# Performance work log

Hardware: AMD Instinct MI355X
Metric: run time of the kernel (lower is better)

Reference implementation:

```python
import jax, jax.numpy as jnp
import numpy as np

FORGET_BIAS = 1.0
LAYERS = 2


def setup_inputs() -> dict:
    key = jax.random.key(0)
    ks = jax.random.split(key, 10)
    B, T, H, V = 64, 50, 256, 50000
    G = 4 * H
    s = 1.0 / np.sqrt(H)
    return {
        "input_data": jax.random.randint(ks[0], (B, T), 0, V, dtype=jnp.int64),
        "embedding": jax.random.uniform(ks[1], (V, H), jnp.float32, -1.0, 1.0),
        "Wx": jax.random.normal(ks[2], (LAYERS, H, G), jnp.float32) * s,
        "Uh": jax.random.normal(ks[3], (LAYERS, H, G), jnp.float32) * s,
        "alpha": jax.random.uniform(ks[4], (LAYERS, G), jnp.float32),
        "beta1": jax.random.uniform(ks[5], (LAYERS, G), jnp.float32),
        "beta2": jax.random.uniform(ks[6], (LAYERS, G), jnp.float32),
        "bias": jnp.zeros((LAYERS, G), jnp.float32),
        "softmax_w": jax.random.normal(ks[7], (V, H), jnp.float32) * s,
        "softmax_b": jnp.full((V,), 0.1, jnp.float32),
    }


def _mi_lstm_stack(inputs_tbh, Wx, Uh, alpha, beta1, beta2, bias):
    # inputs_tbh: [T, B, H]; params have leading layer axis [L, ...]
    T, B, H = inputs_tbh.shape
    c0 = jnp.zeros((LAYERS, B, H), inputs_tbh.dtype)
    h0 = jnp.zeros((LAYERS, B, H), inputs_tbh.dtype)

    def step(carry, x_t):
        c, h = carry
        inp = x_t
        new_c, new_h = [], []
        for l in range(LAYERS):
            xh = inp @ Wx[l]          # [B, 4H]
            hh = h[l] @ Uh[l]         # [B, 4H]
            gates = alpha[l] * xh * hh + beta1[l] * xh + beta2[l] * hh + bias[l]
            i, j, f, o = jnp.split(gates, 4, axis=-1)
            c_l = c[l] * jax.nn.sigmoid(f + FORGET_BIAS) + jax.nn.sigmoid(i) * jnp.tanh(j)
            h_l = jnp.tanh(c_l) * jax.nn.sigmoid(o)
            new_c.append(c_l)
            new_h.append(h_l)
            inp = h_l
        return (jnp.stack(new_c), jnp.stack(new_h)), inp

    (_, _), outs = jax.lax.scan(step, (c0, h0), inputs_tbh)
    return outs  # [T, B, H] top-layer hidden states


def reference(input_data, embedding, Wx, Uh, alpha, beta1, beta2, bias, softmax_w, softmax_b):
    # embedding lookup: [B, T, H] -> time-major [T, B, H]
    x = embedding[input_data]
    outs = _mi_lstm_stack(jnp.transpose(x, (1, 0, 2)), Wx, Uh, alpha, beta1, beta2, bias)
    # batch-major flatten like tf.reshape(outputs, [-1, rnn_size]) on [B, T, H]
    H = outs.shape[-1]
    flat = jnp.transpose(outs, (1, 0, 2)).reshape(-1, H)  # [B*T, H]
    logits = flat @ softmax_w.T + softmax_b               # [B*T, V]
    return logits
```

## Files before the change

### kernel.cpp

```cpp
#include <hip/hip_runtime.h>
#include <hip/hip_bf16.h>
#include <math.h>

#define B_ 64
#define T_ 50
#define H_ 256
#define G_ 1024
#define V_ 50000
#define NBLK 32
#define BSTRIDE 64

using f16x8 = __attribute__((ext_vector_type(8))) _Float16;
using f16x4 = __attribute__((ext_vector_type(4))) _Float16;
using f32x4 = __attribute__((ext_vector_type(4))) float;

__device__ __forceinline__ float sigm(float x) { return 1.0f / (1.0f + expf(-x)); }

__global__ __launch_bounds__(64) void embed_k(const int* __restrict__ idx,
                                              const float* __restrict__ emb,
                                              _Float16* __restrict__ x16)
{
    const int row = blockIdx.x;
    const int b = row & (B_ - 1);
    const int t = row >> 6;
    const int id = idx[b * T_ + t];
    const float4 v = *reinterpret_cast<const float4*>(emb + (size_t)id * H_ + threadIdx.x * 4);
    f16x4 h;
    h[0] = (_Float16)v.x; h[1] = (_Float16)v.y;
    h[2] = (_Float16)v.z; h[3] = (_Float16)v.w;
    *reinterpret_cast<f16x4*>(x16 + (size_t)row * H_ + threadIdx.x * 4) = h;
}

__global__ __launch_bounds__(256) void conv_half(const float* __restrict__ in,
                                                 _Float16* __restrict__ out, int n)
{
    const int i = (blockIdx.x * 256 + threadIdx.x) * 8;
    if (i + 8 <= n) {
        const float4 v0 = *reinterpret_cast<const float4*>(in + i);
        const float4 v1 = *reinterpret_cast<const float4*>(in + i + 4);
        f16x8 h;
        h[0] = (_Float16)v0.x; h[1] = (_Float16)v0.y;
        h[2] = (_Float16)v0.z; h[3] = (_Float16)v0.w;
        h[4] = (_Float16)v1.x; h[5] = (_Float16)v1.y;
        h[6] = (_Float16)v1.z; h[7] = (_Float16)v1.w;
        *reinterpret_cast<f16x8*>(out + i) = h;
    }
}

__global__ __launch_bounds__(256) void pack_wx0(const float* __restrict__ Wx0,
                                                _Float16* __restrict__ wxT)
{
    __shared__ _Float16 ts[64][65];
    const int k0 = blockIdx.x * 64;
    const int n0 = blockIdx.y * 64;
    const int tr = threadIdx.x >> 6;
    const int tc = threadIdx.x & 63;
#pragma unroll
    for (int i = 0; i < 16; ++i) {
        const int r = i * 4 + tr;
        ts[r][tc] = (_Float16)Wx0[(size_t)(k0 + r) * G_ + n0 + tc];
    }
    __syncthreads();
#pragma unroll
    for (int i = 0; i < 16; ++i) {
        const int c = i * 4 + tr;
        wxT[(size_t)(n0 + c) * H_ + k0 + tc] = ts[tc][c];
    }
}

__global__ __launch_bounds__(256) void pack_w_rec(const float* __restrict__ Uh0,
                                                  const float* __restrict__ Wx1,
                                                  const float* __restrict__ Uh1,
                                                  _Float16* __restrict__ wpk)
{
    const int c = blockIdx.x;
    const int m = blockIdx.y;
    const float* __restrict__ src = (m == 0) ? Uh0 : (m == 1) ? Wx1 : Uh1;
    _Float16* __restrict__ dst = wpk + (((size_t)c * 3 + m) << 13);
    for (int i = threadIdx.x; i < 8192; i += 256) {
        const int k = i >> 5;
        const int col = i & 31;
        const int colg = ((col >> 3) << 8) + (c << 3) + (col & 7);
        dst[(col << 8) + k] = (_Float16)src[(size_t)k * G_ + colg];
    }
}

__device__ __forceinline__ void gload_lds16(const void* g, void* l)
{
    __builtin_amdgcn_global_load_lds(
        (const __attribute__((address_space(1))) unsigned int*)g,
        (__attribute__((address_space(3))) unsigned int*)l, 16, 0, 0);
}

__device__ __forceinline__ void gbar_arrive(int* slot)
{
    __syncthreads();
    if (threadIdx.x == 0) {
        __threadfence();
        __hip_atomic_fetch_add(slot, 1, __ATOMIC_RELAXED, __HIP_MEMORY_SCOPE_AGENT);
    }
}

__device__ __forceinline__ void gbar_wait_fast(int* slot)
{
    if (threadIdx.x == 0) {
        while (__hip_atomic_load(slot, __ATOMIC_RELAXED, __HIP_MEMORY_SCOPE_AGENT) < NBLK)
            __builtin_amdgcn_s_sleep(1);
    }
    __syncthreads();
    __threadfence();
}

#define PM 128
#define PN 128
#define PK 64

__global__ __launch_bounds__(256) void gemm16_mfma(
    const _Float16* __restrict__ A16,
    const _Float16* __restrict__ B16,
    float* __restrict__ C)
{
    __shared__ __align__(16) _Float16 Asub[PM * PK];
    __shared__ __align__(16) _Float16 Bsub[PN * PK];

    const int tid = threadIdx.x;
    const int l = tid & 63;
    const int w = tid >> 6;
    const int wm = w >> 1, wn = w & 1;

    const int n0 = blockIdx.x * PN;
    const int m0 = blockIdx.y * PM;

    f32x4 acc[4][4] = {};

    for (int k0 = 0; k0 < H_; k0 += PK) {
#pragma unroll
        for (int is = 0; is < 4; ++is) {
            const int i = is * 256 + tid;
            const int r = i >> 3;
            const int ch = (i & 7) ^ (r & 7);
            gload_lds16(A16 + (size_t)(m0 + r) * H_ + k0 + ch * 8, &Asub[i * 8]);
            gload_lds16(B16 + (size_t)(n0 + r) * H_ + k0 + ch * 8, &Bsub[i * 8]);
        }
        __syncthreads();

#pragma unroll
        for (int ks = 0; ks < 2; ++ks) {
            f16x8 af[4], bf[4];
#pragma unroll
            for (int i = 0; i < 4; ++i) {
                const int r = wm * 64 + i * 16 + (l & 15);
                const int ch = (ks * 4 + (l >> 4)) ^ (r & 7);
                af[i] = *reinterpret_cast<const f16x8*>(&Asub[r * PK + ch * 8]);
            }
#pragma unroll
            for (int jf = 0; jf < 4; ++jf) {
                const int r = wn * 64 + jf * 16 + (l & 15);
                const int ch = (ks * 4 + (l >> 4)) ^ (r & 7);
                bf[jf] = *reinterpret_cast<const f16x8*>(&Bsub[r * PK + ch * 8]);
            }
#pragma unroll
            for (int i = 0; i < 4; ++i)
#pragma unroll
                for (int jf = 0; jf < 4; ++jf)
                    acc[i][jf] = __builtin_amdgcn_mfma_f32_16x16x32_f16(
                        af[i], bf[jf], acc[i][jf], 0, 0, 0);
        }
        __syncthreads();
    }

    const int rb = (l >> 4) << 2;
    const int cl = l & 15;
#pragma unroll
    for (int jf = 0; jf < 4; ++jf) {
        const int col = n0 + wn * 64 + jf * 16 + cl;
#pragma unroll
        for (int i = 0; i < 4; ++i) {
            const int rowb = m0 + wm * 64 + i * 16 + rb;
#pragma unroll
            for (int r = 0; r < 4; ++r)
                C[(size_t)(rowb + r) * G_ + col] = acc[i][jf][r];
        }
    }
}

__global__ __launch_bounds__(256) void mi_rec(
    const _Float16* __restrict__ wpk,
    const float* __restrict__ xh0,
    _Float16* __restrict__ h0x,
    _Float16* __restrict__ h1x,
    _Float16* __restrict__ outsH,
    int* __restrict__ bars,
    const float* __restrict__ alpha, const float* __restrict__ b1,
    const float* __restrict__ b2, const float* __restrict__ bsv)
{
    __shared__ __align__(16) _Float16 h0l[16384];
    __shared__ __align__(16) _Float16 h1l[16384];
    __shared__ __align__(16) _Float16 wl[24576];
    __shared__ float gA[2112], gB[2112];
    __shared__ float c0l[512], c1l[512];

    const int c = blockIdx.x;
    const int tid = threadIdx.x;
    const int l = tid & 63;
    const int w = tid >> 6;

    for (int i = tid; i < 2048; i += 256) {
        *reinterpret_cast<f16x8*>(&h0l[i << 3]) = f16x8{};
        *reinterpret_cast<f16x8*>(&h1l[i << 3]) = f16x8{};
    }
    for (int i = tid; i < 512; i += 256) { c0l[i] = 0.f; c1l[i] = 0.f; }

    for (int i = tid; i < 3072; i += 256) {
        const int m = i >> 10;
        const int col = (i >> 5) & 31;
        const int ch = i & 31;
        const f16x8 v = *reinterpret_cast<const f16x8*>(
            &wpk[(((size_t)c * 3 + m) * 32 + col) * 256 + (ch << 3)]);
        *reinterpret_cast<f16x8*>(
            &wl[(m * 32 + col) * 256 + ((ch ^ (col & 7)) << 3)]) = v;
    }

    const int u = tid & 7, b0 = tid >> 3;
    const int jl = (c << 3) + u;
    float al0[4], b10[4], b20[4], bs0[4], al1[4], b11[4], b21[4], bs1[4];
#pragma unroll
    for (int g = 0; g < 4; ++g) {
        const int col = (g << 8) + jl;
        al0[g] = alpha[col];        b10[g] = b1[col];
        b20[g] = b2[col];           bs0[g] = bsv[col];
        al1[g] = alpha[G_ + col];   b11[g] = b1[G_ + col];
        b21[g] = b2[G_ + col];      bs1[g] = bsv[G_ + col];
    }
    __syncthreads();

    const int arow = (w << 4) + (l & 15);
    const int cA = l & 15, cB = 16 + (l & 15);
    const int kq = l >> 4;

    auto MM = [&](const _Float16* am, const _Float16* bm, f32x4& A0, f32x4& A1) {
#pragma unroll
        for (int s = 0; s < 8; ++s) {
            const int ck = (s << 2) + kq;
            const f16x8 af = *reinterpret_cast<const f16x8*>(
                &am[(arow << 8) + ((ck ^ (arow & 7)) << 3)]);
            const f16x8 bf0 = *reinterpret_cast<const f16x8*>(
                &bm[(cA << 8) + ((ck ^ (cA & 7)) << 3)]);
            const f16x8 bf1 = *reinterpret_cast<const f16x8*>(
                &bm[(cB << 8) + ((ck ^ (cB & 7)) << 3)]);
            A0 = __builtin_amdgcn_mfma_f32_16x16x32_f16(af, bf0, A0, 0, 0, 0);
            A1 = __builtin_amdgcn_mfma_f32_16x16x32_f16(af, bf1, A1, 0, 0, 0);
        }
    };
    auto STG = [&](float* gl, f32x4 A0, f32x4 A1) {
        const int rb = (w << 4) + (kq << 2);
#pragma unroll
        for (int r = 0; r < 4; ++r) {
            gl[(rb + r) * 33 + cA] = A0[r];
            gl[(rb + r) * 33 + cB] = A1[r];
        }
    };
    auto STAGE_H = [&](const _Float16* src, _Float16* dst) {
#pragma unroll
        for (int it = 0; it < 8; ++it) {
            const int idx = (it << 8) + tid;
            const int row = idx >> 5, ch = idx & 31;
            const f16x8 v = *reinterpret_cast<const f16x8*>(&src[(row << 8) + (ch << 3)]);
            *reinterpret_cast<f16x8*>(&dst[(row << 8) + ((ch ^ (row & 7)) << 3)]) = v;
        }
    };

    for (int s = 0; s <= T_; ++s) {
        const int p = s & 1;
        _Float16* h0w = h0x + (p << 14);
        _Float16* h1w = h1x + (p << 14);

        if (s < T_) {
            f32x4 A0 = {}, A1 = {};
            MM(h0l, wl, A0, A1);
            STG(gA, A0, A1);
            __syncthreads();
#pragma unroll
            for (int bb = 0; bb < 2; ++bb) {
                const int b = b0 + (bb << 5);
                float g4[4];
#pragma unroll
                for (int g = 0; g < 4; ++g) {
                    const float a = gA[b * 33 + (g << 3) + u];
                    const float x = xh0[(((size_t)(s * B_ + b)) << 10) + (g << 8) + jl];
                    g4[g] = al0[g] * x * a + b10[g] * x + b20[g] * a + bs0[g];
                }
                const float cn = c0l[(b << 3) + u] * sigm(g4[2] + 1.f)
                               + sigm(g4[0]) * tanhf(g4[1]);
                c0l[(b << 3) + u] = cn;
                h0w[(b << 8) + jl] = (_Float16)(tanhf(cn) * sigm(g4[3]));
            }
            __syncthreads();
        }

        if (s > 0) {
            f32x4 X0 = {}, X1 = {}, H0 = {}, H1 = {};
            MM(h0l, wl + 1 * 8192, X0, X1);
            MM(h1l, wl + 2 * 8192, H0, H1);
            STG(gA, X0, X1);
            STG(gB, H0, H1);
            __syncthreads();
#pragma unroll
            for (int bb = 0; bb < 2; ++bb) {
                const int b = b0 + (bb << 5);
                float g4[4];
#pragma unroll
                for (int g = 0; g < 4; ++g) {
                    const float xa = gA[b * 33 + (g << 3) + u];
                    const float ha = gB[b * 33 + (g << 3) + u];
                    g4[g] = al1[g] * xa * ha + b11[g] * xa + b21[g] * ha + bs1[g];
                }
                const float cn = c1l[(b << 3) + u] * sigm(g4[2] + 1.f)
                               + sigm(g4[0]) * tanhf(g4[1]);
                c1l[(b << 3) + u] = cn;
                const float hn = tanhf(cn) * sigm(g4[3]);
                h1w[(b << 8) + jl] = (_Float16)hn;
                outsH[(((size_t)b * T_ + (s - 1)) << 8) + jl] = (_Float16)hn;
            }
        }

        if (s < T_) {
            gbar_arrive(bars + s * BSTRIDE);
            gbar_wait_fast(bars + s * BSTRIDE);
            STAGE_H(h0w, h0l);
            if (s > 0) STAGE_H(h1w, h1l);
            __syncthreads();
        }
    }
}

__global__ __launch_bounds__(256) void proj_mfma(
    const _Float16* __restrict__ A16,
    const _Float16* __restrict__ B16,
    const float* __restrict__ bias,
    float* __restrict__ C)
{
    __shared__ __align__(16) _Float16 Asub[PM * PK];
    __shared__ __align__(16) _Float16 Bsub[PN * PK];

    const int tid = threadIdx.x;
    const int l = tid & 63;
    const int w = tid >> 6;
    const int wm = w >> 1, wn = w & 1;

    const int m0 = blockIdx.x * PM;
    const int n0 = blockIdx.y * PN;

    f32x4 acc[4][4] = {};

    for (int k0 = 0; k0 < H_; k0 += PK) {
#pragma unroll
        for (int is = 0; is < 4; ++is) {
            const int i = is * 256 + tid;
            const int r = i >> 3;
            const int ch = (i & 7) ^ (r & 7);
            gload_lds16(A16 + (size_t)(m0 + r) * H_ + k0 + ch * 8, &Asub[i * 8]);
            int n = n0 + r; if (n > V_ - 1) n = V_ - 1;
            gload_lds16(B16 + (size_t)n * H_ + k0 + ch * 8, &Bsub[i * 8]);
        }
        __syncthreads();

#pragma unroll
        for (int ks = 0; ks < 2; ++ks) {
            f16x8 af[4], bf[4];
#pragma unroll
            for (int i = 0; i < 4; ++i) {
                const int r = wm * 64 + i * 16 + (l & 15);
                const int ch = (ks * 4 + (l >> 4)) ^ (r & 7);
                af[i] = *reinterpret_cast<const f16x8*>(&Asub[r * PK + ch * 8]);
            }
#pragma unroll
            for (int jf = 0; jf < 4; ++jf) {
                const int r = wn * 64 + jf * 16 + (l & 15);
                const int ch = (ks * 4 + (l >> 4)) ^ (r & 7);
                bf[jf] = *reinterpret_cast<const f16x8*>(&Bsub[r * PK + ch * 8]);
            }
#pragma unroll
            for (int i = 0; i < 4; ++i)
#pragma unroll
                for (int jf = 0; jf < 4; ++jf)
                    acc[i][jf] = __builtin_amdgcn_mfma_f32_16x16x32_f16(
                        af[i], bf[jf], acc[i][jf], 0, 0, 0);
        }
        __syncthreads();
    }

    const int rb = (l >> 4) << 2;
    const int cl = l & 15;
#pragma unroll
    for (int jf = 0; jf < 4; ++jf) {
        const int col = n0 + wn * 64 + jf * 16 + cl;
        if (col < V_) {
            const float bv = bias[col];
#pragma unroll
            for (int i = 0; i < 4; ++i) {
                const int rowb = m0 + wm * 64 + i * 16 + rb;
#pragma unroll
                for (int r = 0; r < 4; ++r)
                    C[(size_t)(rowb + r) * V_ + col] = acc[i][jf][r] + bv;
            }
        }
    }
}

extern "C" void kernel_launch(void* const* d_in, const int* in_sizes, int n_in,
                              void* d_out, int out_size, void* d_ws, size_t ws_size,
                              hipStream_t stream)
{
    const int*   idx   = (const int*)  d_in[0];
    const float* emb   = (const float*)d_in[1];
    const float* Wx    = (const float*)d_in[2];
    const float* Uh    = (const float*)d_in[3];
    const float* alpha = (const float*)d_in[4];
    const float* b1    = (const float*)d_in[5];
    const float* b2    = (const float*)d_in[6];
    const float* bsv   = (const float*)d_in[7];
    const float* sw    = (const float*)d_in[8];
    const float* sb    = (const float*)d_in[9];
    float* out = (float*)d_out;

    char* wsb = (char*)d_ws;
    _Float16* x16   = (_Float16*)(wsb);
    float*    xh0   = (float*)   (wsb + 1638400);
    _Float16* outsH = (_Float16*)(wsb + 14745600);
    _Float16* w16   = (_Float16*)(wsb + 16384000);
    _Float16* wxT   = (_Float16*)(wsb + 41984000);
    _Float16* wpk   = (_Float16*)(wsb + 42508288);
    _Float16* h0x   = (_Float16*)(wsb + 44081152);
    _Float16* h1x   = (_Float16*)(wsb + 44146688);
    int*      bars  = (int*)     (wsb + 44212224);

    const float* Wx0 = Wx;
    const float* Wx1 = Wx + (size_t)H_ * G_;
    const float* Uh0 = Uh;
    const float* Uh1 = Uh + (size_t)H_ * G_;

    (void)hipMemsetAsync(bars, 0, 16384, stream);

    {
        dim3 grid(NBLK, 3);
        pack_w_rec<<<grid, 256, 0, stream>>>(Uh0, Wx1, Uh1, wpk);
    }
    {
        dim3 grid(4, 16);
        pack_wx0<<<grid, 256, 0, stream>>>(Wx0, wxT);
    }
    conv_half<<<(V_ * H_) / 2048, 256, 0, stream>>>(sw, w16, V_ * H_);

    embed_k<<<T_ * B_, 64, 0, stream>>>(idx, emb, x16);

    {
        dim3 grid(G_ / PN, 3200 / PM);
        gemm16_mfma<<<grid, 256, 0, stream>>>(x16, wxT, xh0);
    }

    mi_rec<<<NBLK, 256, 0, stream>>>(wpk, xh0, h0x, h1x, outsH, bars,
                                     alpha, b1, b2, bsv);

    {
        dim3 grid(3200 / PM, (V_ + PN - 1) / PN);
        proj_mfma<<<grid, 256, 0, stream>>>(outsH, w16, sb, out);
    }
}
```

Measured before the change: 751.2 us.

## Exchange recurrent hidden state via packed atomic stores and drop barrier fences

The recurrent kernel now stages each block's hidden-state slice in shared memory, packs pairs of halves into 32-bit words, and publishes them with agent-scope relaxed atomic stores in a block-major layout. Peers read them back with atomic loads straight into the swizzled LDS layout. The explicit threadfences around the grid barrier are removed, and the input-projection loads are hoisted ahead of the matmul. The aim is to shorten the per-timestep cross-block synchronisation latency on the serial critical path. Without the fences, correctness depends on relaxed atomics being visible at agent scope in time, which is a memory-ordering risk.

```diff
diff --git a/kernel.cpp b/kernel.cpp
--- a/kernel.cpp
+++ b/kernel.cpp
@@ -92,25 +92,6 @@
         (__attribute__((address_space(3))) unsigned int*)l, 16, 0, 0);
 }
 
-__device__ __forceinline__ void gbar_arrive(int* slot)
-{
-    __syncthreads();
-    if (threadIdx.x == 0) {
-        __threadfence();
-        __hip_atomic_fetch_add(slot, 1, __ATOMIC_RELAXED, __HIP_MEMORY_SCOPE_AGENT);
-    }
-}
-
-__device__ __forceinline__ void gbar_wait_fast(int* slot)
-{
-    if (threadIdx.x == 0) {
-        while (__hip_atomic_load(slot, __ATOMIC_RELAXED, __HIP_MEMORY_SCOPE_AGENT) < NBLK)
-            __builtin_amdgcn_s_sleep(1);
-    }
-    __syncthreads();
-    __threadfence();
-}
-
 #define PM 128
 #define PN 128
 #define PK 64
@@ -187,8 +168,8 @@
 __global__ __launch_bounds__(256) void mi_rec(
     const _Float16* __restrict__ wpk,
     const float* __restrict__ xh0,
-    _Float16* __restrict__ h0x,
-    _Float16* __restrict__ h1x,
+    unsigned int* __restrict__ h0s,
+    unsigned int* __restrict__ h1s,
     _Float16* __restrict__ outsH,
     int* __restrict__ bars,
     const float* __restrict__ alpha, const float* __restrict__ b1,
@@ -199,6 +180,7 @@
     __shared__ __align__(16) _Float16 wl[24576];
     __shared__ float gA[2112], gB[2112];
     __shared__ float c0l[512], c1l[512];
+    __shared__ _Float16 htmp[512];
 
     const int c = blockIdx.x;
     const int tid = threadIdx.x;
@@ -237,6 +219,8 @@
     const int arow = (w << 4) + (l & 15);
     const int cA = l & 15, cB = 16 + (l & 15);
     const int kq = l >> 4;
+    const int pb = tid >> 2, pq = tid & 3;
+    const unsigned short* htu = reinterpret_cast<const unsigned short*>(htmp);
 
     auto MM = [&](const _Float16* am, const _Float16* bm, f32x4& A0, f32x4& A1) {
 #pragma unroll
@@ -260,22 +244,37 @@
             gl[(rb + r) * 33 + cB] = A1[r];
         }
     };
-    auto STAGE_H = [&](const _Float16* src, _Float16* dst) {
-#pragma unroll
-        for (int it = 0; it < 8; ++it) {
-            const int idx = (it << 8) + tid;
-            const int row = idx >> 5, ch = idx & 31;
-            const f16x8 v = *reinterpret_cast<const f16x8*>(&src[(row << 8) + (ch << 3)]);
-            *reinterpret_cast<f16x8*>(&dst[(row << 8) + ((ch ^ (row & 7)) << 3)]) = v;
+    auto PACK_STORE = [&](unsigned int* dst) {
+        const unsigned int lo = htu[(pb << 3) + (pq << 1)];
+        const unsigned int hi = htu[(pb << 3) + (pq << 1) + 1];
+        __hip_atomic_store(&dst[(c << 8) + tid], lo | (hi << 16),
+                           __ATOMIC_RELAXED, __HIP_MEMORY_SCOPE_AGENT);
+    };
+    auto READ_STAGE = [&](const unsigned int* src, _Float16* dst) {
+#pragma unroll
+        for (int cc = 0; cc < 32; ++cc) {
+            const unsigned int v = __hip_atomic_load(&src[(cc << 8) + tid],
+                                   __ATOMIC_RELAXED, __HIP_MEMORY_SCOPE_AGENT);
+            *reinterpret_cast<unsigned int*>(
+                reinterpret_cast<char*>(dst) + (pb << 9)
+                + ((cc ^ (pb & 7)) << 4) + (pq << 2)) = v;
         }
     };
 
     for (int s = 0; s <= T_; ++s) {
         const int p = s & 1;
-        _Float16* h0w = h0x + (p << 14);
-        _Float16* h1w = h1x + (p << 14);
+        unsigned int* h0d = h0s + (p << 13);
+        unsigned int* h1d = h1s + (p << 13);
 
         if (s < T_) {
+            float xv[2][4];
+#pragma unroll
+            for (int bb = 0; bb < 2; ++bb)
+#pragma unroll
+                for (int g = 0; g < 4; ++g)
+                    xv[bb][g] = xh0[(((size_t)(s * B_ + (b0 + (bb << 5)))) << 10)
+                                    + (g << 8) + jl];
+
             f32x4 A0 = {}, A1 = {};
             MM(h0l, wl, A0, A1);
             STG(gA, A0, A1);
@@ -287,15 +286,16 @@
 #pragma unroll
                 for (int g = 0; g < 4; ++g) {
                     const float a = gA[b * 33 + (g << 3) + u];
-                    const float x = xh0[(((size_t)(s * B_ + b)) << 10) + (g << 8) + jl];
+                    const float x = xv[bb][g];
                     g4[g] = al0[g] * x * a + b10[g] * x + b20[g] * a + bs0[g];
                 }
                 const float cn = c0l[(b << 3) + u] * sigm(g4[2] + 1.f)
                                + sigm(g4[0]) * tanhf(g4[1]);
                 c0l[(b << 3) + u] = cn;
-                h0w[(b << 8) + jl] = (_Float16)(tanhf(cn) * sigm(g4[3]));
-            }
-            __syncthreads();
+                htmp[(b << 3) + u] = (_Float16)(tanhf(cn) * sigm(g4[3]));
+            }
+            __syncthreads();
+            PACK_STORE(h0d);
         }
 
         if (s > 0) {
@@ -319,16 +319,27 @@
                                + sigm(g4[0]) * tanhf(g4[1]);
                 c1l[(b << 3) + u] = cn;
                 const float hn = tanhf(cn) * sigm(g4[3]);
-                h1w[(b << 8) + jl] = (_Float16)hn;
+                htmp[(b << 3) + u] = (_Float16)hn;
                 outsH[(((size_t)b * T_ + (s - 1)) << 8) + jl] = (_Float16)hn;
             }
+            __syncthreads();
+            PACK_STORE(h1d);
         }
 
         if (s < T_) {
-            gbar_arrive(bars + s * BSTRIDE);
-            gbar_wait_fast(bars + s * BSTRIDE);
-            STAGE_H(h0w, h0l);
-            if (s > 0) STAGE_H(h1w, h1l);
+            __syncthreads();
+            if (tid == 0)
+                __hip_atomic_fetch_add(&bars[s * BSTRIDE], 1,
+                                       __ATOMIC_RELAXED, __HIP_MEMORY_SCOPE_AGENT);
+            if (tid == 0) {
+                while (__hip_atomic_load(&bars[s * BSTRIDE],
+                        __ATOMIC_RELAXED, __HIP_MEMORY_SCOPE_AGENT) < NBLK)
+                    __builtin_amdgcn_s_sleep(1);
+            }
+            __syncthreads();
+            asm volatile("" ::: "memory");
+            READ_STAGE(h0s + (p << 13), h0l);
+            if (s > 0) READ_STAGE(h1s + (p << 13), h1l);
             __syncthreads();
         }
     }
@@ -425,15 +436,15 @@
     float* out = (float*)d_out;
 
     char* wsb = (char*)d_ws;
-    _Float16* x16   = (_Float16*)(wsb);
-    float*    xh0   = (float*)   (wsb + 1638400);
-    _Float16* outsH = (_Float16*)(wsb + 14745600);
-    _Float16* w16   = (_Float16*)(wsb + 16384000);
-    _Float16* wxT   = (_Float16*)(wsb + 41984000);
-    _Float16* wpk   = (_Float16*)(wsb + 42508288);
-    _Float16* h0x   = (_Float16*)(wsb + 44081152);
-    _Float16* h1x   = (_Float16*)(wsb + 44146688);
-    int*      bars  = (int*)     (wsb + 44212224);
+    _Float16*     x16   = (_Float16*)    (wsb);
+    float*        xh0   = (float*)       (wsb + 1638400);
+    _Float16*     outsH = (_Float16*)    (wsb + 14745600);
+    _Float16*     w16   = (_Float16*)    (wsb + 16384000);
+    _Float16*     wxT   = (_Float16*)    (wsb + 41984000);
+    _Float16*     wpk   = (_Float16*)    (wsb + 42508288);
+    unsigned int* h0s   = (unsigned int*)(wsb + 44081152);
+    unsigned int* h1s   = (unsigned int*)(wsb + 44146688);
+    int*          bars  = (int*)         (wsb + 44212224);
 
     const float* Wx0 = Wx;
     const float* Wx1 = Wx + (size_t)H_ * G_;
@@ -459,7 +470,7 @@
         gemm16_mfma<<<grid, 256, 0, stream>>>(x16, wxT, xh0);
     }
 
-    mi_rec<<<NBLK, 256, 0, stream>>>(wpk, xh0, h0x, h1x, outsH, bars,
+    mi_rec<<<NBLK, 256, 0, stream>>>(wpk, xh0, h0s, h1s, outsH, bars,
                                      alpha, b1, b2, bsv);
 
     {
```

Result: slower. 1.269 ms (+68.9%).
